# Performance work log

Measured on AMD Instinct MI355X. Metric: run time of the kernel, lower is better.

Reference implementation:

```python
import jax, jax.numpy as jnp
import numpy as np
from jax import lax

B, L = 2, 5000            # images, candidate lines per image
C_IN, C_LOI = 256, 128    # backbone channels, dim_loi
H = W = 256               # feature-map spatial size (indices clamped to 255)
N_PTS0, N_PTS1 = 32, 8    # points sampled per line, after maxpool
POOL = N_PTS0 // N_PTS1   # MaxPool1d kernel/stride = 4
PLANES = C_LOI // 2       # Bottleneck1D mid channels
EPS = 1e-5


def setup_inputs() -> dict:
    key = jax.random.key(0)
    ks = jax.random.split(key, 16)
    f32 = jnp.float32
    s = 0.05
    feature = jax.random.normal(ks[0], (B, C_IN, H, W), f32)
    lines = jax.random.uniform(ks[1], (B, L, 2, 2), f32, minval=0.0, maxval=255.0)
    return {
        "feature": feature,
        "lines": lines,
        "fc1_w": jax.random.normal(ks[2], (C_LOI, C_IN), f32) * s,
        "fc1_b": jnp.zeros((C_LOI,), f32),
        "bn1_g": jnp.ones((C_LOI,), f32),
        "bn1_b": jnp.zeros((C_LOI,), f32),
        "bn1_m": jax.random.normal(ks[3], (C_LOI,), f32) * 0.1,
        "bn1_v": jax.random.uniform(ks[4], (C_LOI,), f32, minval=0.5, maxval=1.5),
        "conv1_w": jax.random.normal(ks[5], (PLANES, C_LOI), f32) * s,
        "conv1_b": jnp.zeros((PLANES,), f32),
        "bn2_g": jnp.ones((PLANES,), f32),
        "bn2_b": jnp.zeros((PLANES,), f32),
        "bn2_m": jax.random.normal(ks[6], (PLANES,), f32) * 0.1,
        "bn2_v": jax.random.uniform(ks[7], (PLANES,), f32, minval=0.5, maxval=1.5),
        "conv2_w": jax.random.normal(ks[8], (PLANES, PLANES, 3), f32) * s,
        "conv2_b": jnp.zeros((PLANES,), f32),
        "bn3_g": jnp.ones((PLANES,), f32),
        "bn3_b": jnp.zeros((PLANES,), f32),
        "bn3_m": jax.random.normal(ks[9], (PLANES,), f32) * 0.1,
        "bn3_v": jax.random.uniform(ks[10], (PLANES,), f32, minval=0.5, maxval=1.5),
        "conv3_w": jax.random.normal(ks[11], (C_LOI, PLANES), f32) * s,
        "conv3_b": jnp.zeros((C_LOI,), f32),
        "fc2_w": jax.random.normal(ks[12], (3, C_LOI * N_PTS1), f32) * s,
        "fc2_b": jnp.zeros((3,), f32),
    }


def _bn(x, g, b, m, v):
    # eval-mode BatchNorm1d over [N, C, T]
    inv = g / jnp.sqrt(v + EPS)
    return x * inv[None, :, None] + (b - m * inv)[None, :, None]


def _bilinear_sample(feat, lines):
    # feat: [B, C, H, W], lines: [B, L, 2, 2] -> [B, L, C, N_PTS0]
    lam = jnp.linspace(0.0, 1.0, N_PTS0, dtype=feat.dtype)[:, None]  # [P,1]
    # p = lam * endpoint0 + (1-lam) * endpoint1 - 0.5  -> [B, L, P, 2]
    p = lines[:, :, 0:1, :] * lam + lines[:, :, 1:2, :] * (1.0 - lam) - 0.5
    px, py = p[..., 0], p[..., 1]                       # [B, L, P]
    px0 = jnp.clip(jnp.floor(px), 0.0, 255.0)
    py0 = jnp.clip(jnp.floor(py), 0.0, 255.0)
    px1 = jnp.clip(px0 + 1.0, 0.0, 255.0)
    py1 = jnp.clip(py0 + 1.0, 0.0, 255.0)
    ix0, iy0 = px0.astype(jnp.int32), py0.astype(jnp.int32)
    ix1, iy1 = px1.astype(jnp.int32), py1.astype(jnp.int32)
    w00 = (px1 - px) * (py1 - py)
    w10 = (px - px0) * (py1 - py)
    w01 = (px1 - px) * (py - py0)
    w11 = (px - px0) * (py - py0)

    def one_image(f, a0, b0, a1, b1, c00, c10, c01, c11):
        # f: [C,H,W], indices/weights: [L,P] -> [C,L,P]
        return (f[:, a0, b0] * c00 + f[:, a1, b0] * c10 +
                f[:, a0, b1] * c01 + f[:, a1, b1] * c11)

    xp = jax.vmap(one_image)(feat, ix0, iy0, ix1, iy1, w00, w10, w01, w11)
    return jnp.transpose(xp, (0, 2, 1, 3))  # [B, L, C, P]


def _forward(feature, lines, fc1_w, fc1_b, bn1_g, bn1_b, bn1_m, bn1_v,
             conv1_w, conv1_b, bn2_g, bn2_b, bn2_m, bn2_v,
             conv2_w, conv2_b, bn3_g, bn3_b, bn3_m, bn3_v,
             conv3_w, conv3_b, fc2_w, fc2_b):
    # fc1: 1x1 conv over the backbone feature map
    x = jnp.einsum('oc,bchw->bohw', fc1_w, feature) + fc1_b[None, :, None, None]
    xp = _bilinear_sample(x, lines)                     # [B, L, C_LOI, P]
    xp = xp.reshape(B * L, C_LOI, N_PTS0)
    # MaxPool1d(kernel=POOL, stride=POOL)
    xp = xp.reshape(B * L, C_LOI, N_PTS1, POOL).max(axis=-1)  # [N, C, T]
    # Bottleneck1D residual branch: BN-ReLU-Conv1(k1)-BN-ReLU-Conv(k3)-BN-ReLU-Conv(k1)
    h = jax.nn.relu(_bn(xp, bn1_g, bn1_b, bn1_m, bn1_v))
    h = jnp.einsum('oc,nct->not', conv1_w, h) + conv1_b[None, :, None]
    h = jax.nn.relu(_bn(h, bn2_g, bn2_b, bn2_m, bn2_v))
    h = lax.conv_general_dilated(h, conv2_w, window_strides=(1,),
                                 padding=((1, 1),),
                                 dimension_numbers=('NCH', 'OIH', 'NCH'))
    h = h + conv2_b[None, :, None]
    h = jax.nn.relu(_bn(h, bn3_g, bn3_b, bn3_m, bn3_v))
    h = jnp.einsum('oc,nct->not', conv3_w, h) + conv3_b[None, :, None]
    xp = xp + h
    # fc2: ReLU + Linear(dim_loi * n_pts1 -> 3)
    flat = jax.nn.relu(xp).reshape(B * L, C_LOI * N_PTS1)
    return flat @ fc2_w.T + fc2_b


def reference(feature, lines, fc1_w, fc1_b, bn1_g, bn1_b, bn1_m, bn1_v,
              conv1_w, conv1_b, bn2_g, bn2_b, bn2_m, bn2_v,
              conv2_w, conv2_b, bn3_g, bn3_b, bn3_m, bn3_v,
              conv3_w, conv3_b, fc2_w, fc2_b):
    return _forward(feature, lines, fc1_w, fc1_b, bn1_g, bn1_b, bn1_m, bn1_v,
                    conv1_w, conv1_b, bn2_g, bn2_b, bn2_m, bn2_v,
                    conv2_w, conv2_b, bn3_g, bn3_b, bn3_m, bn3_v,
                    conv3_w, conv3_b, fc2_w, fc2_b)
```

## Files before the change

kernel.cpp:

```cpp
#include <hip/hip_runtime.h>
#include <hip/hip_bf16.h>

#define BB 2
#define LL 5000
#define CIN 256
#define CLOI 128
#define HH 256
#define WW 256
#define HWP (HH*WW)
#define NPTS0 32
#define NPTS1 8
#define PLANES 64
#define EPSV 1e-5f

#define X_BYTES   ((size_t)BB * HWP * CLOI * 2)
#define XS_BYTES  ((size_t)BB * LL * 1024 * 2)
#define W1S_OFF   (X_BYTES + XS_BYTES)
#define W2S_OFF   (W1S_OFF + 16384)
#define W3S_OFF   (W2S_OFF + 24576)
#define B1P_OFF   (W3S_OFF + 16384)
#define B2P_OFF   (B1P_OFF + 256)
#define S1_OFF    (B2P_OFF + 256)
#define T1_OFF    (S1_OFF + 512)
#define W0S_OFF   (T1_OFF + 512)

typedef unsigned int uint;
typedef unsigned short ushort;
typedef __attribute__((ext_vector_type(8))) short short8;
typedef __attribute__((ext_vector_type(4))) float f32x4;

__device__ __forceinline__ float bf2f(ushort u) {
    uint v = ((uint)u) << 16;
    return __uint_as_float(v);
}
__device__ __forceinline__ ushort f2bf(float f) {
    uint x = __float_as_uint(f);
    uint r = (x + 0x7fffu + ((x >> 16) & 1u)) >> 16;
    return (ushort)r;
}
__device__ __forceinline__ uint pack2(float a, float b) {
    return (uint)f2bf(a) | ((uint)f2bf(b) << 16);
}

__global__ __launch_bounds__(256) void fc1_kernel(
    const float* __restrict__ feature, const ushort* __restrict__ w0s,
    const float* __restrict__ fc1_b, ushort* __restrict__ xout)
{
    __shared__ ushort sF[32 * 64 * 8];

    int tid = threadIdx.x;
    int tile = blockIdx.x;
    int b = tile >> 10;
    int p0 = (tile & 1023) << 6;
    int wv = tid >> 6, lane = tid & 63;
    int q = lane >> 4, ln = lane & 15;

    short8 afr[8][2];
#pragma unroll
    for (int kg = 0; kg < 8; kg++)
#pragma unroll
        for (int mt = 0; mt < 2; mt++)
            afr[kg][mt] = *(const short8*)(w0s + ((size_t)((kg * 4 + q) * 128 + wv * 32 + mt * 16 + ln)) * 8);

    const float* fb = feature + (size_t)b * CIN * HWP + p0;
    int g_ = tid >> 4;
    int qd = tid & 15;
#pragma unroll
    for (int s = 0; s < 2; s++) {
        int g = s * 16 + g_;
        const float* src = fb + (size_t)(g * 8) * HWP + qd * 4;
        float4 rv[8];
#pragma unroll
        for (int j = 0; j < 8; j++) rv[j] = *(const float4*)(src + (size_t)j * HWP);
#pragma unroll
        for (int i = 0; i < 4; i++) {
            uint4 u;
            u.x = pack2(((const float*)&rv[0])[i], ((const float*)&rv[1])[i]);
            u.y = pack2(((const float*)&rv[2])[i], ((const float*)&rv[3])[i]);
            u.z = pack2(((const float*)&rv[4])[i], ((const float*)&rv[5])[i]);
            u.w = pack2(((const float*)&rv[6])[i], ((const float*)&rv[7])[i]);
            *(uint4*)(&sF[(g * 64 + qd * 4 + i) * 8]) = u;
        }
    }
    __syncthreads();

    const f32x4 fzero = { 0.f, 0.f, 0.f, 0.f };
    f32x4 acc[2][4];
#pragma unroll
    for (int mt = 0; mt < 2; mt++)
#pragma unroll
        for (int nt = 0; nt < 4; nt++) acc[mt][nt] = fzero;

#pragma unroll
    for (int kg = 0; kg < 8; kg++) {
#pragma unroll
        for (int nt = 0; nt < 4; nt++) {
            short8 bfr = *(short8*)(&sF[((kg * 4 + q) * 64 + nt * 16 + ln) * 8]);
            acc[0][nt] = __builtin_amdgcn_mfma_f32_16x16x32_bf16(afr[kg][0], bfr, acc[0][nt], 0, 0, 0);
            acc[1][nt] = __builtin_amdgcn_mfma_f32_16x16x32_bf16(afr[kg][1], bfr, acc[1][nt], 0, 0, 0);
        }
    }

    float bias[8];
    *(float4*)bias       = *(const float4*)(fc1_b + wv * 32 + q * 4);
    *(float4*)(bias + 4) = *(const float4*)(fc1_b + wv * 32 + 16 + q * 4);
    ushort* xrow = xout + (size_t)b * HWP * CLOI;
#pragma unroll
    for (int mt = 0; mt < 2; mt++)
#pragma unroll
        for (int nt = 0; nt < 4; nt++) {
            uint2 u;
            u.x = pack2(acc[mt][nt][0] + bias[mt * 4 + 0], acc[mt][nt][1] + bias[mt * 4 + 1]);
            u.y = pack2(acc[mt][nt][2] + bias[mt * 4 + 2], acc[mt][nt][3] + bias[mt * 4 + 3]);
            *(uint2*)(xrow + (size_t)(p0 + nt * 16 + ln) * CLOI + wv * 32 + mt * 16 + q * 4) = u;
        }
}

__global__ __launch_bounds__(256) void prep_kernel(
    const float* __restrict__ conv1_w, const float* __restrict__ conv1_b,
    const float* __restrict__ bn2_g, const float* __restrict__ bn2_b,
    const float* __restrict__ bn2_m, const float* __restrict__ bn2_v,
    const float* __restrict__ conv2_w, const float* __restrict__ conv2_b,
    const float* __restrict__ bn3_g, const float* __restrict__ bn3_b,
    const float* __restrict__ bn3_m, const float* __restrict__ bn3_v,
    const float* __restrict__ conv3_w,
    const float* __restrict__ bn1_g, const float* __restrict__ bn1_b,
    const float* __restrict__ bn1_m, const float* __restrict__ bn1_v,
    const float* __restrict__ fc1_w,
    ushort* __restrict__ w1s, ushort* __restrict__ w2s, ushort* __restrict__ w3s,
    float* __restrict__ b1p, float* __restrict__ b2p,
    float* __restrict__ s1o, float* __restrict__ t1o,
    ushort* __restrict__ w0s)
{
    int idx = blockIdx.x * 256 + threadIdx.x;
    if (idx < 8192) {
        int kg = idx >> 9, rem = idx & 511, m = rem >> 3, j = rem & 7;
        int c = kg * 8 + j;
        float s2 = bn2_g[m] * rsqrtf(bn2_v[m] + EPSV);
        w1s[idx] = f2bf(conv1_w[m * 128 + c] * s2);
    }
    if (idx < 12288) {
        int dt = idx >> 12, rem = idx & 4095;
        int kg = rem >> 9, m = (rem >> 3) & 63, j = rem & 7;
        int i = kg * 8 + j;
        float s3 = bn3_g[m] * rsqrtf(bn3_v[m] + EPSV);
        w2s[idx] = f2bf(conv2_w[m * 192 + i * 3 + dt] * s3);
    }
    if (idx < 8192) {
        int kg = idx >> 10, rem = idx & 1023, m = rem >> 3, j = rem & 7;
        w3s[idx] = f2bf(conv3_w[m * 64 + kg * 8 + j]);
    }
    if (idx < 32768) {
        int grp = idx >> 10, rem = idx & 1023, m = rem >> 3, j = rem & 7;
        w0s[idx] = f2bf(fc1_w[m * CIN + grp * 8 + j]);
    }
    if (idx < 64) {
        float s2 = bn2_g[idx] * rsqrtf(bn2_v[idx] + EPSV);
        b1p[idx] = conv1_b[idx] * s2 + bn2_b[idx] - bn2_m[idx] * s2;
        float s3 = bn3_g[idx] * rsqrtf(bn3_v[idx] + EPSV);
        b2p[idx] = conv2_b[idx] * s3 + bn3_b[idx] - bn3_m[idx] * s3;
    }
    if (idx < 128) {
        float s1 = bn1_g[idx] * rsqrtf(bn1_v[idx] + EPSV);
        s1o[idx] = s1;
        t1o[idx] = bn1_b[idx] - bn1_m[idx] * s1;
    }
}

__global__ __launch_bounds__(256) void sample_kernel(
    const ushort* __restrict__ x, const float* __restrict__ lines,
    ushort* __restrict__ xsb)
{
    __shared__ int   sIdx[NPTS0][4];
    __shared__ float sWt[NPTS0][4];

    int n = blockIdx.x;
    int b = n / LL;
    int tid = threadIdx.x;

    if (tid < NPTS0) {
        int j = tid;
        float lam = (float)j * (1.0f / 31.0f);
        const float* lp = lines + (size_t)n * 4;
        float e0x = lp[0], e0y = lp[1], e1x = lp[2], e1y = lp[3];
        float px = e0x * lam + e1x * (1.f - lam) - 0.5f;
        float py = e0y * lam + e1y * (1.f - lam) - 0.5f;
        float px0 = fminf(fmaxf(floorf(px), 0.f), 255.f);
        float py0 = fminf(fmaxf(floorf(py), 0.f), 255.f);
        float px1 = fminf(px0 + 1.f, 255.f);
        float py1 = fminf(py0 + 1.f, 255.f);
        int ix0 = (int)px0, iy0 = (int)py0, ix1 = (int)px1, iy1 = (int)py1;
        sIdx[j][0] = ix0 * WW + iy0;
        sIdx[j][1] = ix1 * WW + iy0;
        sIdx[j][2] = ix0 * WW + iy1;
        sIdx[j][3] = ix1 * WW + iy1;
        sWt[j][0] = (px1 - px) * (py1 - py);
        sWt[j][1] = (px - px0) * (py1 - py);
        sWt[j][2] = (px1 - px) * (py - py0);
        sWt[j][3] = (px - px0) * (py - py0);
    }
    __syncthreads();

    int w = tid >> 6, lane = tid & 63;
    const uint* xb = (const uint*)(x + (size_t)b * HWP * CLOI);

    float m00 = -INFINITY, m10 = -INFINITY;
    float m01 = -INFINITY, m11 = -INFINITY;

#pragma unroll
    for (int jj = 0; jj < 8; jj++) {
        int j = w * 8 + jj;
        int i00 = sIdx[j][0], i10 = sIdx[j][1], i01 = sIdx[j][2], i11 = sIdx[j][3];
        float w00 = sWt[j][0], w10 = sWt[j][1], w01 = sWt[j][2], w11 = sWt[j][3];
        uint u00 = xb[(size_t)i00 * 64 + lane];
        uint u10 = xb[(size_t)i10 * 64 + lane];
        uint u01 = xb[(size_t)i01 * 64 + lane];
        uint u11 = xb[(size_t)i11 * 64 + lane];
        float v0 = bf2f((ushort)(u00 & 0xffff)) * w00 + bf2f((ushort)(u10 & 0xffff)) * w10
                 + bf2f((ushort)(u01 & 0xffff)) * w01 + bf2f((ushort)(u11 & 0xffff)) * w11;
        float v1 = bf2f((ushort)(u00 >> 16)) * w00 + bf2f((ushort)(u10 >> 16)) * w10
                 + bf2f((ushort)(u01 >> 16)) * w01 + bf2f((ushort)(u11 >> 16)) * w11;
        if (jj < 4) { m00 = fmaxf(m00, v0); m10 = fmaxf(m10, v1); }
        else        { m01 = fmaxf(m01, v0); m11 = fmaxf(m11, v1); }
    }

    ushort* basep = xsb + (size_t)n * 1024;
    int kg = lane >> 2;
    int j2 = (lane & 3) * 2;
    *(uint*)(basep + kg * 64 + (2 * w) * 8 + j2) = pack2(m00, m10);
    *(uint*)(basep + kg * 64 + (2 * w + 1) * 8 + j2) = pack2(m01, m11);
}

__global__ __launch_bounds__(256) void head_kernel(
    const ushort* __restrict__ xsb,
    const ushort* __restrict__ w1s, const ushort* __restrict__ w2s,
    const ushort* __restrict__ w3s,
    const float* __restrict__ b1p, const float* __restrict__ b2p,
    const float* __restrict__ s1g, const float* __restrict__ t1g,
    const float* __restrict__ conv3_b,
    const float* __restrict__ fc2_w, const float* __restrict__ fc2_b,
    float* __restrict__ out)
{
    __shared__ ushort sXS[8192];
    __shared__ ushort sH1[8192];
    __shared__ ushort sB2[4096];
    __shared__ float  sFC2[3072];
    __shared__ float  sS1[128], sT1[128];
    __shared__ float  sB1[64], sB2b[64], sB3b[128];

    int tid = threadIdx.x;
    int wv = tid >> 6, lane = tid & 63;
    int q = lane >> 4, ln = lane & 15;
    int L0 = blockIdx.x * 8;
    int colg = wv * 16 + ln;

    if (tid < 128) { sS1[tid] = s1g[tid]; sT1[tid] = t1g[tid]; sB3b[tid] = conv3_b[tid]; }
    if (tid < 64)  { sB1[tid] = b1p[tid]; sB2b[tid] = b2p[tid]; }
#pragma unroll
    for (int it = 0; it < 12; it++) sFC2[it * 256 + tid] = fc2_w[it * 256 + tid];
    __syncthreads();

#pragma unroll
    for (int it = 0; it < 4; it++) {
        int ch = it * 256 + tid;
        int l = ch >> 7, wc = ch & 127;
        int kg = wc >> 3, tt = wc & 7;
        int col = l * 8 + tt;
        uint4 raw = *(const uint4*)(xsb + (size_t)(L0 + l) * 1024 + wc * 8);
        int off = (kg * 64 + col) * 8;
        *(uint4*)(&sXS[off]) = raw;
        uint rw[4] = { raw.x, raw.y, raw.z, raw.w };
        uint hw[4];
#pragma unroll
        for (int p = 0; p < 4; p++) {
            int c = kg * 8 + p * 2;
            float v0 = bf2f((ushort)(rw[p] & 0xffff));
            float v1 = bf2f((ushort)(rw[p] >> 16));
            float h0 = fmaxf(v0 * sS1[c] + sT1[c], 0.f);
            float h1v = fmaxf(v1 * sS1[c + 1] + sT1[c + 1], 0.f);
            hw[p] = pack2(h0, h1v);
        }
        uint4 hv; hv.x = hw[0]; hv.y = hw[1]; hv.z = hw[2]; hv.w = hw[3];
        *(uint4*)(&sH1[off]) = hv;
    }
    __syncthreads();

    const short8 bzero = { 0, 0, 0, 0, 0, 0, 0, 0 };
    const f32x4 fzero = { 0.f, 0.f, 0.f, 0.f };

    f32x4 acc1[4];
#pragma unroll
    for (int mt = 0; mt < 4; mt++) acc1[mt] = fzero;
#pragma unroll
    for (int ks = 0; ks < 4; ks++) {
        short8 b = *(short8*)(&sH1[((ks * 4 + q) * 64 + colg) * 8]);
#pragma unroll
        for (int mt = 0; mt < 4; mt++) {
            short8 a = *(const short8*)(w1s + ((ks * 4 + q) * 64 + mt * 16 + ln) * 8);
            acc1[mt] = __builtin_amdgcn_mfma_f32_16x16x32_bf16(a, b, acc1[mt], 0, 0, 0);
        }
    }
#pragma unroll
    for (int mt = 0; mt < 4; mt++) {
        int m0 = mt * 16 + q * 4;
        float v0 = fmaxf(acc1[mt][0] + sB1[m0 + 0], 0.f);
        float v1 = fmaxf(acc1[mt][1] + sB1[m0 + 1], 0.f);
        float v2 = fmaxf(acc1[mt][2] + sB1[m0 + 2], 0.f);
        float v3 = fmaxf(acc1[mt][3] + sB1[m0 + 3], 0.f);
        uint2 u; u.x = pack2(v0, v1); u.y = pack2(v2, v3);
        *(uint2*)(&sB2[((m0 >> 3) * 64 + colg) * 8 + (m0 & 7)]) = u;
    }
    __syncthreads();

    f32x4 acc2[4];
#pragma unroll
    for (int mt = 0; mt < 4; mt++) acc2[mt] = fzero;
    int tpos = colg & 7;
#pragma unroll
    for (int dt = 0; dt < 3; dt++) {
        int tsh = tpos + dt - 1;
        bool valid = ((unsigned)tsh < 8u);
        int colr = colg + dt - 1;
        colr = colr < 0 ? 0 : (colr > 63 ? 63 : colr);
#pragma unroll
        for (int ks = 0; ks < 2; ks++) {
            short8 b = *(short8*)(&sB2[((ks * 4 + q) * 64 + colr) * 8]);
            b = valid ? b : bzero;
#pragma unroll
            for (int mt = 0; mt < 4; mt++) {
                short8 a = *(const short8*)(w2s + dt * 4096 + ((ks * 4 + q) * 64 + mt * 16 + ln) * 8);
                acc2[mt] = __builtin_amdgcn_mfma_f32_16x16x32_bf16(a, b, acc2[mt], 0, 0, 0);
            }
        }
    }
#pragma unroll
    for (int mt = 0; mt < 4; mt++) {
        int m0 = mt * 16 + q * 4;
        float v0 = fmaxf(acc2[mt][0] + sB2b[m0 + 0], 0.f);
        float v1 = fmaxf(acc2[mt][1] + sB2b[m0 + 1], 0.f);
        float v2 = fmaxf(acc2[mt][2] + sB2b[m0 + 2], 0.f);
        float v3 = fmaxf(acc2[mt][3] + sB2b[m0 + 3], 0.f);
        uint2 u; u.x = pack2(v0, v1); u.y = pack2(v2, v3);
        *(uint2*)(&sH1[((m0 >> 3) * 64 + colg) * 8 + (m0 & 7)]) = u;
    }
    __syncthreads();

    f32x4 acc3[8];
#pragma unroll
    for (int mt = 0; mt < 8; mt++) acc3[mt] = fzero;
#pragma unroll
    for (int ks = 0; ks < 2; ks++) {
        short8 b = *(short8*)(&sH1[((ks * 4 + q) * 64 + colg) * 8]);
#pragma unroll
        for (int mt = 0; mt < 8; mt++) {
            short8 a = *(const short8*)(w3s + ((ks * 4 + q) * 128 + mt * 16 + ln) * 8);
            acc3[mt] = __builtin_amdgcn_mfma_f32_16x16x32_bf16(a, b, acc3[mt], 0, 0, 0);
        }
    }

    float p0 = 0.f, p1 = 0.f, p2 = 0.f;
#pragma unroll
    for (int mt = 0; mt < 8; mt++) {
#pragma unroll
        for (int r = 0; r < 4; r++) {
            int m = mt * 16 + q * 4 + r;
            float xsv = bf2f(sXS[(m >> 3) * 512 + colg * 8 + (m & 7)]);
            float v = fmaxf(xsv + acc3[mt][r] + sB3b[m], 0.f);
            int fi = m * 8 + tpos;
            p0 += v * sFC2[fi];
            p1 += v * sFC2[1024 + fi];
            p2 += v * sFC2[2048 + fi];
        }
    }
    p0 += __shfl_xor(p0, 32); p1 += __shfl_xor(p1, 32); p2 += __shfl_xor(p2, 32);
    p0 += __shfl_xor(p0, 16); p1 += __shfl_xor(p1, 16); p2 += __shfl_xor(p2, 16);
    p0 += __shfl_xor(p0, 4);  p1 += __shfl_xor(p1, 4);  p2 += __shfl_xor(p2, 4);
    p0 += __shfl_xor(p0, 2);  p1 += __shfl_xor(p1, 2);  p2 += __shfl_xor(p2, 2);
    p0 += __shfl_xor(p0, 1);  p1 += __shfl_xor(p1, 1);  p2 += __shfl_xor(p2, 1);

    if (lane == 0 || lane == 8) {
        int line = L0 + wv * 2 + (lane >> 3);
        out[(size_t)line * 3 + 0] = p0 + fc2_b[0];
        out[(size_t)line * 3 + 1] = p1 + fc2_b[1];
        out[(size_t)line * 3 + 2] = p2 + fc2_b[2];
    }
}

extern "C" void kernel_launch(void* const* d_in, const int* in_sizes, int n_in,
                              void* d_out, int out_size, void* d_ws, size_t ws_size,
                              hipStream_t stream) {
    const float* feature = (const float*)d_in[0];
    const float* lines   = (const float*)d_in[1];
    const float* fc1_w   = (const float*)d_in[2];
    const float* fc1_b   = (const float*)d_in[3];
    const float* bn1_g   = (const float*)d_in[4];
    const float* bn1_b   = (const float*)d_in[5];
    const float* bn1_m   = (const float*)d_in[6];
    const float* bn1_v   = (const float*)d_in[7];
    const float* conv1_w = (const float*)d_in[8];
    const float* conv1_b = (const float*)d_in[9];
    const float* bn2_g   = (const float*)d_in[10];
    const float* bn2_b   = (const float*)d_in[11];
    const float* bn2_m   = (const float*)d_in[12];
    const float* bn2_v   = (const float*)d_in[13];
    const float* conv2_w = (const float*)d_in[14];
    const float* conv2_b = (const float*)d_in[15];
    const float* bn3_g   = (const float*)d_in[16];
    const float* bn3_b   = (const float*)d_in[17];
    const float* bn3_m   = (const float*)d_in[18];
    const float* bn3_v   = (const float*)d_in[19];
    const float* conv3_w = (const float*)d_in[20];
    const float* conv3_b = (const float*)d_in[21];
    const float* fc2_w   = (const float*)d_in[22];
    const float* fc2_b   = (const float*)d_in[23];
    float* out = (float*)d_out;

    char* ws = (char*)d_ws;
    ushort* x_bf = (ushort*)ws;
    ushort* xs_b = (ushort*)(ws + X_BYTES);
    ushort* w1s  = (ushort*)(ws + W1S_OFF);
    ushort* w2s  = (ushort*)(ws + W2S_OFF);
    ushort* w3s  = (ushort*)(ws + W3S_OFF);
    float*  b1p  = (float*)(ws + B1P_OFF);
    float*  b2p  = (float*)(ws + B2P_OFF);
    float*  s1g  = (float*)(ws + S1_OFF);
    float*  t1g  = (float*)(ws + T1_OFF);
    ushort* w0s  = (ushort*)(ws + W0S_OFF);

    prep_kernel<<<128, 256, 0, stream>>>(
        conv1_w, conv1_b, bn2_g, bn2_b, bn2_m, bn2_v,
        conv2_w, conv2_b, bn3_g, bn3_b, bn3_m, bn3_v,
        conv3_w, bn1_g, bn1_b, bn1_m, bn1_v, fc1_w,
        w1s, w2s, w3s, b1p, b2p, s1g, t1g, w0s);
    fc1_kernel<<<2048, 256, 0, stream>>>(feature, w0s, fc1_b, x_bf);
    sample_kernel<<<BB * LL, 256, 0, stream>>>(x_bf, lines, xs_b);
    head_kernel<<<BB * LL / 8, 256, 0, stream>>>(
        xs_b, w1s, w2s, w3s, b1p, b2p, s1g, t1g, conv3_b, fc2_w, fc2_b, out);
}
```

Baseline: 299.1 us.

## Fuse bilinear sampling into head kernel and swizzle LDS layout

Merges the separate sample and head kernels into one kernel that samples 8 lines per block directly into shared memory. This drops the global round-trip of the pooled features and one kernel launch. It also XOR-swizzles the LDS layout to reduce bank conflicts and reads fc2 weights from global memory instead of staging them in LDS, which frees shared memory for a launch-bounds occupancy hint of 3. The trade-off is fewer, larger blocks (1250 instead of 10000), each running a serial 8-line gather loop, which may leave the gathers with less latency hiding.

```diff
diff --git a/kernel.cpp b/kernel.cpp
--- a/kernel.cpp
+++ b/kernel.cpp
@@ -167,72 +167,8 @@
     }
 }
 
-__global__ __launch_bounds__(256) void sample_kernel(
+__global__ __launch_bounds__(256, 3) void sample_head_kernel(
     const ushort* __restrict__ x, const float* __restrict__ lines,
-    ushort* __restrict__ xsb)
-{
-    __shared__ int   sIdx[NPTS0][4];
-    __shared__ float sWt[NPTS0][4];
-
-    int n = blockIdx.x;
-    int b = n / LL;
-    int tid = threadIdx.x;
-
-    if (tid < NPTS0) {
-        int j = tid;
-        float lam = (float)j * (1.0f / 31.0f);
-        const float* lp = lines + (size_t)n * 4;
-        float e0x = lp[0], e0y = lp[1], e1x = lp[2], e1y = lp[3];
-        float px = e0x * lam + e1x * (1.f - lam) - 0.5f;
-        float py = e0y * lam + e1y * (1.f - lam) - 0.5f;
-        float px0 = fminf(fmaxf(floorf(px), 0.f), 255.f);
-        float py0 = fminf(fmaxf(floorf(py), 0.f), 255.f);
-        float px1 = fminf(px0 + 1.f, 255.f);
-        float py1 = fminf(py0 + 1.f, 255.f);
-        int ix0 = (int)px0, iy0 = (int)py0, ix1 = (int)px1, iy1 = (int)py1;
-        sIdx[j][0] = ix0 * WW + iy0;
-        sIdx[j][1] = ix1 * WW + iy0;
-        sIdx[j][2] = ix0 * WW + iy1;
-        sIdx[j][3] = ix1 * WW + iy1;
-        sWt[j][0] = (px1 - px) * (py1 - py);
-        sWt[j][1] = (px - px0) * (py1 - py);
-        sWt[j][2] = (px1 - px) * (py - py0);
-        sWt[j][3] = (px - px0) * (py - py0);
-    }
-    __syncthreads();
-
-    int w = tid >> 6, lane = tid & 63;
-    const uint* xb = (const uint*)(x + (size_t)b * HWP * CLOI);
-
-    float m00 = -INFINITY, m10 = -INFINITY;
-    float m01 = -INFINITY, m11 = -INFINITY;
-
-#pragma unroll
-    for (int jj = 0; jj < 8; jj++) {
-        int j = w * 8 + jj;
-        int i00 = sIdx[j][0], i10 = sIdx[j][1], i01 = sIdx[j][2], i11 = sIdx[j][3];
-        float w00 = sWt[j][0], w10 = sWt[j][1], w01 = sWt[j][2], w11 = sWt[j][3];
-        uint u00 = xb[(size_t)i00 * 64 + lane];
-        uint u10 = xb[(size_t)i10 * 64 + lane];
-        uint u01 = xb[(size_t)i01 * 64 + lane];
-        uint u11 = xb[(size_t)i11 * 64 + lane];
-        float v0 = bf2f((ushort)(u00 & 0xffff)) * w00 + bf2f((ushort)(u10 & 0xffff)) * w10
-                 + bf2f((ushort)(u01 & 0xffff)) * w01 + bf2f((ushort)(u11 & 0xffff)) * w11;
-        float v1 = bf2f((ushort)(u00 >> 16)) * w00 + bf2f((ushort)(u10 >> 16)) * w10
-                 + bf2f((ushort)(u01 >> 16)) * w01 + bf2f((ushort)(u11 >> 16)) * w11;
-        if (jj < 4) { m00 = fmaxf(m00, v0); m10 = fmaxf(m10, v1); }
-        else        { m01 = fmaxf(m01, v0); m11 = fmaxf(m11, v1); }
-    }
-
-    ushort* basep = xsb + (size_t)n * 1024;
-    int kg = lane >> 2;
-    int j2 = (lane & 3) * 2;
-    *(uint*)(basep + kg * 64 + (2 * w) * 8 + j2) = pack2(m00, m10);
-    *(uint*)(basep + kg * 64 + (2 * w + 1) * 8 + j2) = pack2(m01, m11);
-}
-
-__global__ __launch_bounds__(256) void head_kernel(
-    const ushort* __restrict__ xsb,
     const ushort* __restrict__ w1s, const ushort* __restrict__ w2s,
     const ushort* __restrict__ w3s,
     const float* __restrict__ b1p, const float* __restrict__ b2p,
@@ -244,44 +180,78 @@
     __shared__ ushort sXS[8192];
     __shared__ ushort sH1[8192];
     __shared__ ushort sB2[4096];
-    __shared__ float  sFC2[3072];
-    __shared__ float  sS1[128], sT1[128];
-    __shared__ float  sB1[64], sB2b[64], sB3b[128];
+    __shared__ int   sIdx[8][32][4];
+    __shared__ float sWt[8][32][4];
+    __shared__ float sB1[64], sB2b[64], sB3b[128];
 
     int tid = threadIdx.x;
     int wv = tid >> 6, lane = tid & 63;
     int q = lane >> 4, ln = lane & 15;
     int L0 = blockIdx.x * 8;
+    int b = L0 / LL;
     int colg = wv * 16 + ln;
 
-    if (tid < 128) { sS1[tid] = s1g[tid]; sT1[tid] = t1g[tid]; sB3b[tid] = conv3_b[tid]; }
+    if (tid < 128) sB3b[tid] = conv3_b[tid];
     if (tid < 64)  { sB1[tid] = b1p[tid]; sB2b[tid] = b2p[tid]; }
-#pragma unroll
-    for (int it = 0; it < 12; it++) sFC2[it * 256 + tid] = fc2_w[it * 256 + tid];
+
+    float s1a = s1g[2 * lane], s1c = s1g[2 * lane + 1];
+    float t1a = t1g[2 * lane], t1c = t1g[2 * lane + 1];
+
+    {
+        int l = tid >> 5, j = tid & 31;
+        float lam = (float)j * (1.0f / 31.0f);
+        const float* lp = lines + (size_t)(L0 + l) * 4;
+        float e0x = lp[0], e0y = lp[1], e1x = lp[2], e1y = lp[3];
+        float px = e0x * lam + e1x * (1.f - lam) - 0.5f;
+        float py = e0y * lam + e1y * (1.f - lam) - 0.5f;
+        float px0 = fminf(fmaxf(floorf(px), 0.f), 255.f);
+        float py0 = fminf(fmaxf(floorf(py), 0.f), 255.f);
+        float px1 = fminf(px0 + 1.f, 255.f);
+        float py1 = fminf(py0 + 1.f, 255.f);
+        int ix0 = (int)px0, iy0 = (int)py0, ix1 = (int)px1, iy1 = (int)py1;
+        sIdx[l][j][0] = ix0 * WW + iy0;
+        sIdx[l][j][1] = ix1 * WW + iy0;
+        sIdx[l][j][2] = ix0 * WW + iy1;
+        sIdx[l][j][3] = ix1 * WW + iy1;
+        sWt[l][j][0] = (px1 - px) * (py1 - py);
+        sWt[l][j][1] = (px - px0) * (py1 - py);
+        sWt[l][j][2] = (px1 - px) * (py - py0);
+        sWt[l][j][3] = (px - px0) * (py - py0);
+    }
     __syncthreads();
 
-#pragma unroll
-    for (int it = 0; it < 4; it++) {
-        int ch = it * 256 + tid;
-        int l = ch >> 7, wc = ch & 127;
-        int kg = wc >> 3, tt = wc & 7;
-        int col = l * 8 + tt;
-        uint4 raw = *(const uint4*)(xsb + (size_t)(L0 + l) * 1024 + wc * 8);
-        int off = (kg * 64 + col) * 8;
-        *(uint4*)(&sXS[off]) = raw;
-        uint rw[4] = { raw.x, raw.y, raw.z, raw.w };
-        uint hw[4];
-#pragma unroll
-        for (int p = 0; p < 4; p++) {
-            int c = kg * 8 + p * 2;
-            float v0 = bf2f((ushort)(rw[p] & 0xffff));
-            float v1 = bf2f((ushort)(rw[p] >> 16));
-            float h0 = fmaxf(v0 * sS1[c] + sT1[c], 0.f);
-            float h1v = fmaxf(v1 * sS1[c + 1] + sT1[c + 1], 0.f);
-            hw[p] = pack2(h0, h1v);
-        }
-        uint4 hv; hv.x = hw[0]; hv.y = hw[1]; hv.z = hw[2]; hv.w = hw[3];
-        *(uint4*)(&sH1[off]) = hv;
+    const uint* xb = (const uint*)(x + (size_t)b * HWP * CLOI);
+    int kg = lane >> 2;
+    int j2 = (lane & 3) * 2;
+    int swz = (kg & 7) << 3;
+
+    for (int l = 0; l < 8; l++) {
+        float m00 = -INFINITY, m10 = -INFINITY;
+        float m01 = -INFINITY, m11 = -INFINITY;
+#pragma unroll
+        for (int jj = 0; jj < 8; jj++) {
+            int j = wv * 8 + jj;
+            int i00 = sIdx[l][j][0], i10 = sIdx[l][j][1], i01 = sIdx[l][j][2], i11 = sIdx[l][j][3];
+            float w00 = sWt[l][j][0], w10 = sWt[l][j][1], w01 = sWt[l][j][2], w11 = sWt[l][j][3];
+            uint u00 = xb[(size_t)i00 * 64 + lane];
+            uint u10 = xb[(size_t)i10 * 64 + lane];
+            uint u01 = xb[(size_t)i01 * 64 + lane];
+            uint u11 = xb[(size_t)i11 * 64 + lane];
+            float v0 = bf2f((ushort)(u00 & 0xffff)) * w00 + bf2f((ushort)(u10 & 0xffff)) * w10
+                     + bf2f((ushort)(u01 & 0xffff)) * w01 + bf2f((ushort)(u11 & 0xffff)) * w11;
+            float v1 = bf2f((ushort)(u00 >> 16)) * w00 + bf2f((ushort)(u10 >> 16)) * w10
+                     + bf2f((ushort)(u01 >> 16)) * w01 + bf2f((ushort)(u11 >> 16)) * w11;
+            if (jj < 4) { m00 = fmaxf(m00, v0); m10 = fmaxf(m10, v1); }
+            else        { m01 = fmaxf(m01, v0); m11 = fmaxf(m11, v1); }
+        }
+        int col0 = l * 8 + 2 * wv;
+        int base0 = (kg * 64 + col0) * 8 + j2;
+        *(uint*)(&sXS[base0 ^ swz])       = pack2(m00, m10);
+        *(uint*)(&sXS[(base0 + 8) ^ swz]) = pack2(m01, m11);
+        float h00 = fmaxf(m00 * s1a + t1a, 0.f), h10 = fmaxf(m10 * s1c + t1c, 0.f);
+        float h01 = fmaxf(m01 * s1a + t1a, 0.f), h11 = fmaxf(m11 * s1c + t1c, 0.f);
+        *(uint*)(&sH1[base0 ^ swz])       = pack2(h00, h10);
+        *(uint*)(&sH1[(base0 + 8) ^ swz]) = pack2(h01, h11);
     }
     __syncthreads();
 
@@ -293,11 +263,12 @@
     for (int mt = 0; mt < 4; mt++) acc1[mt] = fzero;
 #pragma unroll
     for (int ks = 0; ks < 4; ks++) {
-        short8 b = *(short8*)(&sH1[((ks * 4 + q) * 64 + colg) * 8]);
+        int kk = ks * 4 + q;
+        short8 bfrag = *(short8*)(&sH1[((kk * 64 + colg) * 8) ^ ((kk & 7) << 3)]);
 #pragma unroll
         for (int mt = 0; mt < 4; mt++) {
-            short8 a = *(const short8*)(w1s + ((ks * 4 + q) * 64 + mt * 16 + ln) * 8);
-            acc1[mt] = __builtin_amdgcn_mfma_f32_16x16x32_bf16(a, b, acc1[mt], 0, 0, 0);
+            short8 a = *(const short8*)(w1s + (kk * 64 + mt * 16 + ln) * 8);
+            acc1[mt] = __builtin_amdgcn_mfma_f32_16x16x32_bf16(a, bfrag, acc1[mt], 0, 0, 0);
         }
     }
 #pragma unroll
@@ -324,12 +295,13 @@
         colr = colr < 0 ? 0 : (colr > 63 ? 63 : colr);
 #pragma unroll
         for (int ks = 0; ks < 2; ks++) {
-            short8 b = *(short8*)(&sB2[((ks * 4 + q) * 64 + colr) * 8]);
-            b = valid ? b : bzero;
+            int kk = ks * 4 + q;
+            short8 bfrag = *(short8*)(&sB2[(kk * 64 + colr) * 8]);
+            bfrag = valid ? bfrag : bzero;
 #pragma unroll
             for (int mt = 0; mt < 4; mt++) {
-                short8 a = *(const short8*)(w2s + dt * 4096 + ((ks * 4 + q) * 64 + mt * 16 + ln) * 8);
-                acc2[mt] = __builtin_amdgcn_mfma_f32_16x16x32_bf16(a, b, acc2[mt], 0, 0, 0);
+                short8 a = *(const short8*)(w2s + dt * 4096 + (kk * 64 + mt * 16 + ln) * 8);
+                acc2[mt] = __builtin_amdgcn_mfma_f32_16x16x32_bf16(a, bfrag, acc2[mt], 0, 0, 0);
             }
         }
     }
@@ -341,7 +313,8 @@
         float v2 = fmaxf(acc2[mt][2] + sB2b[m0 + 2], 0.f);
         float v3 = fmaxf(acc2[mt][3] + sB2b[m0 + 3], 0.f);
         uint2 u; u.x = pack2(v0, v1); u.y = pack2(v2, v3);
-        *(uint2*)(&sH1[((m0 >> 3) * 64 + colg) * 8 + (m0 & 7)]) = u;
+        int idx = ((m0 >> 3) * 64 + colg) * 8 + (m0 & 7);
+        *(uint2*)(&sH1[idx ^ (((m0 >> 3) & 7) << 3)]) = u;
     }
     __syncthreads();
 
@@ -350,11 +323,12 @@
     for (int mt = 0; mt < 8; mt++) acc3[mt] = fzero;
 #pragma unroll
     for (int ks = 0; ks < 2; ks++) {
-        short8 b = *(short8*)(&sH1[((ks * 4 + q) * 64 + colg) * 8]);
+        int kk = ks * 4 + q;
+        short8 bfrag = *(short8*)(&sH1[((kk * 64 + colg) * 8) ^ ((kk & 7) << 3)]);
 #pragma unroll
         for (int mt = 0; mt < 8; mt++) {
-            short8 a = *(const short8*)(w3s + ((ks * 4 + q) * 128 + mt * 16 + ln) * 8);
-            acc3[mt] = __builtin_amdgcn_mfma_f32_16x16x32_bf16(a, b, acc3[mt], 0, 0, 0);
+            short8 a = *(const short8*)(w3s + (kk * 128 + mt * 16 + ln) * 8);
+            acc3[mt] = __builtin_amdgcn_mfma_f32_16x16x32_bf16(a, bfrag, acc3[mt], 0, 0, 0);
         }
     }
 
@@ -364,12 +338,13 @@
 #pragma unroll
         for (int r = 0; r < 4; r++) {
             int m = mt * 16 + q * 4 + r;
-            float xsv = bf2f(sXS[(m >> 3) * 512 + colg * 8 + (m & 7)]);
+            int idx = ((m >> 3) * 512 + colg * 8 + (m & 7)) ^ (((m >> 3) & 7) << 3);
+            float xsv = bf2f(sXS[idx]);
             float v = fmaxf(xsv + acc3[mt][r] + sB3b[m], 0.f);
             int fi = m * 8 + tpos;
-            p0 += v * sFC2[fi];
-            p1 += v * sFC2[1024 + fi];
-            p2 += v * sFC2[2048 + fi];
+            p0 += v * fc2_w[fi];
+            p1 += v * fc2_w[1024 + fi];
+            p2 += v * fc2_w[2048 + fi];
         }
     }
     p0 += __shfl_xor(p0, 32); p1 += __shfl_xor(p1, 32); p2 += __shfl_xor(p2, 32);
@@ -417,7 +392,6 @@
 
     char* ws = (char*)d_ws;
     ushort* x_bf = (ushort*)ws;
-    ushort* xs_b = (ushort*)(ws + X_BYTES);
     ushort* w1s  = (ushort*)(ws + W1S_OFF);
     ushort* w2s  = (ushort*)(ws + W2S_OFF);
     ushort* w3s  = (ushort*)(ws + W3S_OFF);
@@ -433,7 +407,6 @@
         conv3_w, bn1_g, bn1_b, bn1_m, bn1_v, fc1_w,
         w1s, w2s, w3s, b1p, b2p, s1g, t1g, w0s);
     fc1_kernel<<<2048, 256, 0, stream>>>(feature, w0s, fc1_b, x_bf);
-    sample_kernel<<<BB * LL, 256, 0, stream>>>(x_bf, lines, xs_b);
-    head_kernel<<<BB * LL / 8, 256, 0, stream>>>(
-        xs_b, w1s, w2s, w3s, b1p, b2p, s1g, t1g, conv3_b, fc2_w, fc2_b, out);
-}
+    sample_head_kernel<<<BB * LL / 8, 256, 0, stream>>>(
+        x_bf, lines, w1s, w2s, w3s, b1p, b2p, s1g, t1g, conv3_b, fc2_w, fc2_b, out);
+}
```

Measured after the change: 291.8 us. 2.5% less time.
